# Performance work log

Hardware: AMD Instinct MI355X
Metric: run time of the kernel (lower is better)

The kernel has to match this reference:

```python
import jax, jax.numpy as jnp
import numpy as np

B, S, LATENT = 256, 64, 20
U_DIM = LATENT // 5            # 4
T_HID, T_DEPTH = 20, 4         # treatment MLP
D_HID, D_DEPTH = 4 * LATENT, 4 # drift MLP (80 hidden)
T_LEN = 41
DT = 0.05
SIGMA, THETA, MU = 0.5, 1.0, 0.0
N = B * S
DIM_AUG = LATENT + 2           # latent + logqp + Tx


def _mlp(x, w_in, b_in, w_h, b_h, w_out, b_out, act):
    # input layer always ReLU (MLPSimple), hidden layers use `act`
    h = jax.nn.relu(x @ w_in.T + b_in)
    for i in range(w_h.shape[0]):
        h = act(h @ w_h[i].T + b_h[i])
    return h @ w_out.T + b_out


def setup_inputs() -> dict:
    key = jax.random.key(0)
    ks = jax.random.split(key, 20)

    def lin(k, out_d, in_d):
        bound = 1.0 / np.sqrt(in_d)
        return jax.random.uniform(k, (out_d, in_d), jnp.float32, -bound, bound)

    def bias(k, out_d, in_d):
        bound = 1.0 / np.sqrt(in_d)
        return jax.random.uniform(k, (out_d,), jnp.float32, -bound, bound)

    return {
        "z_SDE": jax.random.normal(ks[0], (B, S, LATENT), jnp.float32),
        "t": jnp.arange(T_LEN, dtype=jnp.float32) * DT,
        "Tx": jax.random.uniform(ks[1], (B,), jnp.float32),
        "noise": jax.random.normal(ks[2], (T_LEN - 1, N, DIM_AUG), jnp.float32),
        # treatment MLP: 1 -> 20 (ReLU) -> [20->20 ReLU]x4 -> 4
        "tw_in": lin(ks[3], T_HID, 1),
        "tb_in": bias(ks[4], T_HID, 1),
        "tw_h": jnp.stack([lin(jax.random.fold_in(ks[5], i), T_HID, T_HID) for i in range(T_DEPTH)]),
        "tb_h": jnp.stack([bias(jax.random.fold_in(ks[6], i), T_HID, T_HID) for i in range(T_DEPTH)]),
        "tw_out": lin(ks[7], U_DIM, T_HID),
        "tb_out": bias(ks[8], U_DIM, T_HID),
        # drift MLP: 24 -> 80 (ReLU) -> [80->80 Tanh]x4 -> 20
        "dw_in": lin(ks[9], D_HID, LATENT + U_DIM),
        "db_in": bias(ks[10], D_HID, LATENT + U_DIM),
        "dw_h": jnp.stack([lin(jax.random.fold_in(ks[11], i), D_HID, D_HID) for i in range(D_DEPTH)]),
        "db_h": jnp.stack([bias(jax.random.fold_in(ks[12], i), D_HID, D_HID) for i in range(D_DEPTH)]),
        "dw_out": lin(ks[13], LATENT, D_HID),
        "db_out": bias(ks[14], LATENT, D_HID),
    }


def reference(z_SDE, t, Tx, noise, tw_in, tb_in, tw_h, tb_h, tw_out, tb_out,
              dw_in, db_in, dw_h, db_h, dw_out, db_out):
    # build augmented initial state: [z, logqp0=0, Tx]  -> [N, DIM_AUG]
    Tx_rep = jnp.broadcast_to(Tx[:, None, None], (B, S, 1))
    aug_y0 = jnp.concatenate(
        [z_SDE, jnp.zeros((B, S, 1), z_SDE.dtype), Tx_rep.astype(z_SDE.dtype)], axis=-1
    ).reshape(N, DIM_AUG)

    dt = t[1] - t[0]           # 0.05, aligned with euler dt
    sqrt_dt = jnp.sqrt(dt)
    # diagonal diffusion: sigma on latent dims, 0 on (logqp, Tx) aug dims
    g_diag = jnp.concatenate([jnp.full((LATENT,), SIGMA, jnp.float32), jnp.zeros((2,), jnp.float32)])

    def f_aug(ti, y_aug):
        T_ = y_aug[:, -1]                     # treatment indicator
        y = y_aug[:, :LATENT]
        t_col = jnp.broadcast_to(ti, (N, 1)).astype(y.dtype)
        u = _mlp(t_col, tw_in, tb_in, tw_h, tb_h, tw_out, tb_out, jax.nn.relu)
        u_t = u * T_[:, None]
        h = THETA * (MU - y)                  # prior drift
        f = _mlp(jnp.concatenate([y, u_t], axis=-1), dw_in, db_in, dw_h, db_h, dw_out, db_out, jnp.tanh) - h
        # _stable_division(f - h, g); g = sigma = 0.5 > eps so plain division
        uu = (f - h) / SIGMA
        f_logqp = 0.5 * jnp.sum(uu * uu, axis=1, keepdims=True)
        return jnp.concatenate([f, f_logqp, jnp.zeros_like(f_logqp)], axis=1)

    def step(y, inp):
        ti, dW = inp
        y_new = y + f_aug(ti, y) * dt + g_diag[None, :] * (dW * sqrt_dt)
        return y_new, y_new

    _, ys_rest = jax.lax.scan(step, aug_y0, (t[:-1], noise))
    aug_ys = jnp.concatenate([aug_y0[None], ys_rest], axis=0)   # [T, N, DIM_AUG]
    # faithful to source: raw reshape of [T, N, dim] into [B, S, T, dim]
    aug_ys = aug_ys.reshape(-1, S, T_LEN, DIM_AUG)
    ys = aug_ys[:, :, :, :-2]
    logqp = aug_ys[:, :, -1, -2]
    return ys, logqp
```

## Files before the change

### kernel.cpp

```cpp
#include <hip/hip_runtime.h>
#include <math.h>
#include <stdint.h>

#define NPART 16384
#define NSTEP 40
#define DIMA  22
#define OUT0_ELEMS 13434880
#define TRAJ_OFF   160

typedef __attribute__((ext_vector_type(8))) short short8;
typedef __attribute__((ext_vector_type(4))) float floatx4;
typedef __attribute__((ext_vector_type(4))) int   intx4;
typedef __attribute__((ext_vector_type(2))) int   intx2;

union V4 { intx4 i; short8 s; floatx4 f; };

#define AIN_B   0
#define AH_B    5120
#define AOUT_B  56320
#define U_B     61440
#define LDS_BYTES 62080
#define STAGE_DW  15360

__device__ __forceinline__ uint32_t bf16r(float x) {
    uint32_t u = __float_as_uint(x);
    u += 0x7FFFu + ((u >> 16) & 1u);
    return u >> 16;
}
__device__ __forceinline__ uint32_t pk2(float a0, float a1) {
    return bf16r(a0) | (bf16r(a1) << 16);
}
__device__ __forceinline__ float fast_tanh(float x) {
    float e = __expf(2.0f * x);
    return 1.0f - 2.0f * __builtin_amdgcn_rcpf(e + 1.0f);
}

__global__ __launch_bounds__(256, 1) void sde_mfma(
    const float* __restrict__ z,      const float* __restrict__ t_arr,
    const float* __restrict__ Tx,     const float* __restrict__ noise,
    const float* __restrict__ dw_in,  const float* __restrict__ db_in,
    const float* __restrict__ dw_h,   const float* __restrict__ db_h,
    const float* __restrict__ dw_out, const float* __restrict__ db_out,
    const float* __restrict__ tw_in,  const float* __restrict__ tb_in,
    const float* __restrict__ tw_h,   const float* __restrict__ tb_h,
    const float* __restrict__ tw_out, const float* __restrict__ tb_out,
    float* __restrict__ out0,         float* __restrict__ traj)
{
    __shared__ __align__(16) uint8_t lds[LDS_BYTES];
    const int tid = threadIdx.x;

    for (int di = tid; di < STAGE_DW; di += 256) {
        uint32_t val = 0u;
        if (di < 1280) {
            int r = di & 255, lane = r >> 2, w = r & 3;
            int m = lane & 15, q = lane >> 4, mt = di >> 8;
            int f = -1;
            if (w < 2)            f = 4 * q + 2 * w;
            else if (q == 0)      f = 16 + 2 * (w - 2);
            else if (q == 1)      f = 20 + 2 * (w - 2);
            if (f >= 0) val = pk2(dw_in[(mt * 16 + m) * 24 + f],
                                  dw_in[(mt * 16 + m) * 24 + f + 1]);
        } else if (di < 14080) {
            int q2 = di - 1280, g = q2 / 640, r = q2 % 640;
            int l = g / 5, mt = g % 5;
            int lane, f;
            if (r < 512) {
                int kt = r >> 8, rr = r & 255, w = rr & 3;
                lane = rr >> 2;
                f = 16 * (2 * kt + (w >> 1)) + 4 * (lane >> 4) + 2 * (w & 1);
            } else {
                int rr = r - 512, d = rr & 1;
                lane = rr >> 1;
                f = 64 + 4 * (lane >> 4) + 2 * d;
            }
            int m = lane & 15;
            val = pk2(dw_h[l * 6400 + (mt * 16 + m) * 80 + f],
                      dw_h[l * 6400 + (mt * 16 + m) * 80 + f + 1]);
        } else {
            int q2 = di - 14080, mt = q2 / 640, r = q2 % 640;
            int lane, f;
            if (r < 512) {
                int kt = r >> 8, rr = r & 255, w = rr & 3;
                lane = rr >> 2;
                f = 16 * (2 * kt + (w >> 1)) + 4 * (lane >> 4) + 2 * (w & 1);
            } else {
                int rr = r - 512, d = rr & 1;
                lane = rr >> 1;
                f = 64 + 4 * (lane >> 4) + 2 * d;
            }
            int m = mt * 16 + (lane & 15);
            if (m < 20) val = pk2(dw_out[m * 80 + f], dw_out[m * 80 + f + 1]);
        }
        ((uint32_t*)lds)[di] = val;
    }
    if (tid < NSTEP) {
        float ti = t_arr[tid];
        float hh[20], h2[20];
        #pragma unroll
        for (int j = 0; j < 20; j++) {
            float v = tw_in[j] * ti + tb_in[j];
            hh[j] = v > 0.f ? v : 0.f;
        }
        #pragma unroll
        for (int l = 0; l < 4; l++) {
            #pragma unroll
            for (int j = 0; j < 20; j++) {
                float a = tb_h[l * 20 + j];
                #pragma unroll
                for (int k = 0; k < 20; k++) a += tw_h[(l * 20 + j) * 20 + k] * hh[k];
                h2[j] = a > 0.f ? a : 0.f;
            }
            #pragma unroll
            for (int j = 0; j < 20; j++) hh[j] = h2[j];
        }
        #pragma unroll
        for (int c = 0; c < 4; c++) {
            float a = tb_out[c];
            #pragma unroll
            for (int k = 0; k < 20; k++) a += tw_out[c * 20 + k] * hh[k];
            ((float*)(lds + U_B))[tid * 4 + c] = a;
        }
    }

    const int lane = tid & 63;
    const int n15  = lane & 15;
    const int quad = lane >> 4;
    const int wv   = tid >> 6;
    const int n    = blockIdx.x * 64 + wv * 16 + n15;
    const float Txb = Tx[blockIdx.x];
    const float dtv = t_arr[1] - t_arr[0];
    const float sdt = sqrtf(dtv);

    floatx4 cIn[5], cH[4][5], cOut[2];
    #pragma unroll
    for (int mt = 0; mt < 5; mt++)
        cIn[mt] = *(const floatx4*)(db_in + mt * 16 + quad * 4);
    #pragma unroll
    for (int l = 0; l < 4; l++)
        #pragma unroll
        for (int mt = 0; mt < 5; mt++)
            cH[l][mt] = *(const floatx4*)(db_h + l * 80 + mt * 16 + quad * 4);
    cOut[0] = *(const floatx4*)(db_out + quad * 4);
    cOut[1] = (quad == 0) ? *(const floatx4*)(db_out + 16)
                          : (floatx4){0.f, 0.f, 0.f, 0.f};
    __syncthreads();

    float y0[4], y1[4] = {0.f, 0.f, 0.f, 0.f};
    {
        floatx4 zv = *(const floatx4*)(z + (size_t)n * 20 + quad * 4);
        #pragma unroll
        for (int r = 0; r < 4; r++) y0[r] = zv[r];
        *(floatx4*)(out0 + (size_t)n * 20 + quad * 4) = zv;
        if (quad == 0) {
            floatx4 z2 = *(const floatx4*)(z + (size_t)n * 20 + 16);
            #pragma unroll
            for (int r = 0; r < 4; r++) y1[r] = z2[r];
            *(floatx4*)(out0 + (size_t)n * 20 + 16) = z2;
            traj[n] = 0.f;
        }
    }

    double lq = 0.0;
    for (int i = 0; i < NSTEP; i++) {
        size_t nbase = ((size_t)i * NPART + n) * DIMA;
        floatx4 dW0 = *(const floatx4*)(noise + nbase + quad * 4);
        floatx4 dW1 = {0.f, 0.f, 0.f, 0.f};
        if (quad == 0) dW1 = *(const floatx4*)(noise + nbase + 16);

        const float* su = (const float*)(lds + U_B) + i * 4;
        float ut0 = su[0] * Txb, ut1 = su[1] * Txb;
        float ut2 = su[2] * Txb, ut3 = su[3] * Txb;

        V4 bin;
        bin.i[0] = pk2(y0[0], y0[1]);
        bin.i[1] = pk2(y0[2], y0[3]);
        if (quad == 0)      { bin.i[2] = pk2(y1[0], y1[1]); bin.i[3] = pk2(y1[2], y1[3]); }
        else if (quad == 1) { bin.i[2] = pk2(ut0, ut1);     bin.i[3] = pk2(ut2, ut3); }
        else                { bin.i[2] = 0;                 bin.i[3] = 0; }

        floatx4 acc[5];
        #pragma unroll
        for (int mt = 0; mt < 5; mt++) {
            V4 a; a.i = *(const intx4*)(lds + AIN_B + mt * 1024 + lane * 16);
            acc[mt] = __builtin_amdgcn_mfma_f32_16x16x32_bf16(a.s, bin.s, cIn[mt], 0, 0, 0);
        }
        uint32_t pkA[5][2];
        #pragma unroll
        for (int mt = 0; mt < 5; mt++) {
            pkA[mt][0] = pk2(fmaxf(acc[mt][0], 0.f), fmaxf(acc[mt][1], 0.f));
            pkA[mt][1] = pk2(fmaxf(acc[mt][2], 0.f), fmaxf(acc[mt][3], 0.f));
        }

        #pragma unroll
        for (int l = 0; l < 4; l++) {
            V4 b0, b1, b2;
            b0.i = (intx4){(int)pkA[0][0], (int)pkA[0][1], (int)pkA[1][0], (int)pkA[1][1]};
            b1.i = (intx4){(int)pkA[2][0], (int)pkA[2][1], (int)pkA[3][0], (int)pkA[3][1]};
            b2.i = (intx4){(int)pkA[4][0], (int)pkA[4][1], 0, 0};
            #pragma unroll
            for (int mt = 0; mt < 5; mt++) {
                const uint8_t* grp = lds + AH_B + (size_t)(l * 5 + mt) * 2560;
                V4 a0; a0.i = *(const intx4*)(grp + lane * 16);
                V4 a1; a1.i = *(const intx4*)(grp + 1024 + lane * 16);
                intx2 h2 = *(const intx2*)(grp + 2048 + lane * 8);
                V4 a2; a2.i = (intx4){h2[0], h2[1], 0, 0};
                floatx4 c = cH[l][mt];
                c = __builtin_amdgcn_mfma_f32_16x16x32_bf16(a0.s, b0.s, c, 0, 0, 0);
                c = __builtin_amdgcn_mfma_f32_16x16x32_bf16(a1.s, b1.s, c, 0, 0, 0);
                c = __builtin_amdgcn_mfma_f32_16x16x32_bf16(a2.s, b2.s, c, 0, 0, 0);
                acc[mt] = c;
            }
            #pragma unroll
            for (int mt = 0; mt < 5; mt++) {
                pkA[mt][0] = pk2(fast_tanh(acc[mt][0]), fast_tanh(acc[mt][1]));
                pkA[mt][1] = pk2(fast_tanh(acc[mt][2]), fast_tanh(acc[mt][3]));
            }
        }

        V4 b0, b1, b2;
        b0.i = (intx4){(int)pkA[0][0], (int)pkA[0][1], (int)pkA[1][0], (int)pkA[1][1]};
        b1.i = (intx4){(int)pkA[2][0], (int)pkA[2][1], (int)pkA[3][0], (int)pkA[3][1]};
        b2.i = (intx4){(int)pkA[4][0], (int)pkA[4][1], 0, 0};
        floatx4 oacc[2];
        #pragma unroll
        for (int mt = 0; mt < 2; mt++) {
            const uint8_t* grp = lds + AOUT_B + (size_t)mt * 2560;
            V4 a0; a0.i = *(const intx4*)(grp + lane * 16);
            V4 a1; a1.i = *(const intx4*)(grp + 1024 + lane * 16);
            intx2 h2 = *(const intx2*)(grp + 2048 + lane * 8);
            V4 a2; a2.i = (intx4){h2[0], h2[1], 0, 0};
            floatx4 c = cOut[mt];
            c = __builtin_amdgcn_mfma_f32_16x16x32_bf16(a0.s, b0.s, c, 0, 0, 0);
            c = __builtin_amdgcn_mfma_f32_16x16x32_bf16(a1.s, b1.s, c, 0, 0, 0);
            oacc[mt] = __builtin_amdgcn_mfma_f32_16x16x32_bf16(a2.s, b2.s, c, 0, 0, 0);
        }

        float part = 0.f;
        size_t obase = ((size_t)(i + 1) * NPART + n) * 20;
        floatx4 st;
        #pragma unroll
        for (int r = 0; r < 4; r++) {
            float o = oacc[0][r];
            float y = y0[r];
            float f = o + y;
            float uu = 2.f * o + 4.f * y;
            part += uu * uu;
            y0[r] = y + f * dtv + (0.5f * sdt) * dW0[r];
            st[r] = y0[r];
        }
        *(floatx4*)(out0 + obase + quad * 4) = st;
        if (quad == 0) {
            floatx4 st2;
            #pragma unroll
            for (int r = 0; r < 4; r++) {
                float o = oacc[1][r];
                float y = y1[r];
                float f = o + y;
                float uu = 2.f * o + 4.f * y;
                part += uu * uu;
                y1[r] = y + f * dtv + (0.5f * sdt) * dW1[r];
                st2[r] = y1[r];
            }
            *(floatx4*)(out0 + obase + 16) = st2;
        }
        part += __shfl_xor(part, 16);
        part += __shfl_xor(part, 32);
        lq += 0.5 * (double)part * (double)dtv;
        if (quad == 0) traj[(size_t)(i + 1) * NPART + n] = (float)lq;
    }
}

__global__ void gather_logqp(const float* __restrict__ traj, float* __restrict__ out1) {
    int i = blockIdx.x * 256 + threadIdx.x;
    if (i < NPART) out1[i] = traj[(size_t)41 * i + 40];
}

extern "C" void kernel_launch(void* const* d_in, const int* in_sizes, int n_in,
                              void* d_out, int out_size, void* d_ws, size_t ws_size,
                              hipStream_t stream) {
    const float* z      = (const float*)d_in[0];
    const float* t_arr  = (const float*)d_in[1];
    const float* Tx     = (const float*)d_in[2];
    const float* noise  = (const float*)d_in[3];
    const float* tw_in  = (const float*)d_in[4];
    const float* tb_in  = (const float*)d_in[5];
    const float* tw_h   = (const float*)d_in[6];
    const float* tb_h   = (const float*)d_in[7];
    const float* tw_out = (const float*)d_in[8];
    const float* tb_out = (const float*)d_in[9];
    const float* dw_in  = (const float*)d_in[10];
    const float* db_in  = (const float*)d_in[11];
    const float* dw_h   = (const float*)d_in[12];
    const float* db_h   = (const float*)d_in[13];
    const float* dw_out = (const float*)d_in[14];
    const float* db_out = (const float*)d_in[15];

    float* wsf  = (float*)d_ws;
    float* traj = wsf + TRAJ_OFF;
    float* out0 = (float*)d_out;
    float* out1 = out0 + OUT0_ELEMS;

    hipLaunchKernelGGL(sde_mfma, dim3(256), dim3(256), 0, stream,
                       z, t_arr, Tx, noise, dw_in, db_in, dw_h, db_h,
                       dw_out, db_out, tw_in, tb_in, tw_h, tb_h, tw_out, tb_out,
                       out0, traj);
    hipLaunchKernelGGL(gather_logqp, dim3(64), dim3(256), 0, stream, traj, out1);
}
```

Before: 274.8 us.

## Prefetch next layer weights from LDS, move biases to LDS, use packed bf16 convert

Bias vectors now live in LDS instead of about 88 persistent registers. The next MLP layer's weight fragments and biases are prefetched from LDS while the current layer's tanh is computed, so LDS latency overlaps with ALU work. The input-layer weights stay in registers across the time loop. The bf16 packing uses the hardware packed-convert builtin when it is available. This trades register pressure for extra LDS reads per step, and the packed convert may round differently in edge cases.

```diff
diff --git a/kernel.cpp b/kernel.cpp
--- a/kernel.cpp
+++ b/kernel.cpp
@@ -18,8 +18,8 @@
 #define AIN_B   0
 #define AH_B    5120
 #define AOUT_B  56320
-#define U_B     61440
-#define LDS_BYTES 62080
+#define SB_B    62080
+#define LDS_BYTES 64448
 #define STAGE_DW  15360
 
 __device__ __forceinline__ uint32_t bf16r(float x) {
@@ -29,6 +29,20 @@
 }
 __device__ __forceinline__ uint32_t pk2(float a0, float a1) {
     return bf16r(a0) | (bf16r(a1) << 16);
+}
+#if defined(__has_builtin)
+#if __has_builtin(__builtin_amdgcn_cvt_pk_bf16_f32)
+#define HAS_PKCVT 1
+#endif
+#endif
+__device__ __forceinline__ uint32_t pkq(float a0, float a1) {
+#ifdef HAS_PKCVT
+    auto r = __builtin_amdgcn_cvt_pk_bf16_f32(a0, a1);
+    uint32_t u; __builtin_memcpy(&u, &r, 4);
+    return u;
+#else
+    return pk2(a0, a1);
+#endif
 }
 __device__ __forceinline__ float fast_tanh(float x) {
     float e = __expf(2.0f * x);
@@ -93,32 +107,42 @@
         }
         ((uint32_t*)lds)[di] = val;
     }
-    if (tid < NSTEP) {
-        float ti = t_arr[tid];
-        float hh[20], h2[20];
-        #pragma unroll
-        for (int j = 0; j < 20; j++) {
-            float v = tw_in[j] * ti + tb_in[j];
-            hh[j] = v > 0.f ? v : 0.f;
-        }
-        #pragma unroll
-        for (int l = 0; l < 4; l++) {
+    {
+        float* sb = (float*)(lds + SB_B);
+        for (int di = tid; di < 432; di += 256) {
+            float v;
+            if (di < 80)       v = db_in[di];
+            else if (di < 400) v = db_h[di - 80];
+            else               v = (di - 400 < 20) ? db_out[di - 400] : 0.f;
+            sb[di] = v;
+        }
+        if (tid < NSTEP) {
+            float ti = t_arr[tid];
+            float hh[20], h2[20];
             #pragma unroll
             for (int j = 0; j < 20; j++) {
-                float a = tb_h[l * 20 + j];
-                #pragma unroll
-                for (int k = 0; k < 20; k++) a += tw_h[(l * 20 + j) * 20 + k] * hh[k];
-                h2[j] = a > 0.f ? a : 0.f;
-            }
-            #pragma unroll
-            for (int j = 0; j < 20; j++) hh[j] = h2[j];
-        }
-        #pragma unroll
-        for (int c = 0; c < 4; c++) {
-            float a = tb_out[c];
-            #pragma unroll
-            for (int k = 0; k < 20; k++) a += tw_out[c * 20 + k] * hh[k];
-            ((float*)(lds + U_B))[tid * 4 + c] = a;
+                float v = tw_in[j] * ti + tb_in[j];
+                hh[j] = v > 0.f ? v : 0.f;
+            }
+            #pragma unroll
+            for (int l = 0; l < 4; l++) {
+                #pragma unroll
+                for (int j = 0; j < 20; j++) {
+                    float a = tb_h[l * 20 + j];
+                    #pragma unroll
+                    for (int k = 0; k < 20; k++) a += tw_h[(l * 20 + j) * 20 + k] * hh[k];
+                    h2[j] = a > 0.f ? a : 0.f;
+                }
+                #pragma unroll
+                for (int j = 0; j < 20; j++) hh[j] = h2[j];
+            }
+            #pragma unroll
+            for (int c = 0; c < 4; c++) {
+                float a = tb_out[c];
+                #pragma unroll
+                for (int k = 0; k < 20; k++) a += tw_out[c * 20 + k] * hh[k];
+                sb[432 + tid * 4 + c] = a;
+            }
         }
     }
 
@@ -130,20 +154,13 @@
     const float Txb = Tx[blockIdx.x];
     const float dtv = t_arr[1] - t_arr[0];
     const float sdt = sqrtf(dtv);
-
-    floatx4 cIn[5], cH[4][5], cOut[2];
+    const float* sbf = (const float*)(lds + SB_B);
+    __syncthreads();
+
+    V4 aIn[5];
     #pragma unroll
     for (int mt = 0; mt < 5; mt++)
-        cIn[mt] = *(const floatx4*)(db_in + mt * 16 + quad * 4);
-    #pragma unroll
-    for (int l = 0; l < 4; l++)
-        #pragma unroll
-        for (int mt = 0; mt < 5; mt++)
-            cH[l][mt] = *(const floatx4*)(db_h + l * 80 + mt * 16 + quad * 4);
-    cOut[0] = *(const floatx4*)(db_out + quad * 4);
-    cOut[1] = (quad == 0) ? *(const floatx4*)(db_out + 16)
-                          : (floatx4){0.f, 0.f, 0.f, 0.f};
-    __syncthreads();
+        aIn[mt].i = *(const intx4*)(lds + AIN_B + mt * 1024 + lane * 16);
 
     float y0[4], y1[4] = {0.f, 0.f, 0.f, 0.f};
     {
@@ -167,30 +184,39 @@
         floatx4 dW1 = {0.f, 0.f, 0.f, 0.f};
         if (quad == 0) dW1 = *(const floatx4*)(noise + nbase + 16);
 
-        const float* su = (const float*)(lds + U_B) + i * 4;
-        float ut0 = su[0] * Txb, ut1 = su[1] * Txb;
-        float ut2 = su[2] * Txb, ut3 = su[3] * Txb;
+        float ut0 = sbf[432 + i * 4 + 0] * Txb, ut1 = sbf[432 + i * 4 + 1] * Txb;
+        float ut2 = sbf[432 + i * 4 + 2] * Txb, ut3 = sbf[432 + i * 4 + 3] * Txb;
 
         V4 bin;
-        bin.i[0] = pk2(y0[0], y0[1]);
-        bin.i[1] = pk2(y0[2], y0[3]);
-        if (quad == 0)      { bin.i[2] = pk2(y1[0], y1[1]); bin.i[3] = pk2(y1[2], y1[3]); }
-        else if (quad == 1) { bin.i[2] = pk2(ut0, ut1);     bin.i[3] = pk2(ut2, ut3); }
+        bin.i[0] = pkq(y0[0], y0[1]);
+        bin.i[1] = pkq(y0[2], y0[3]);
+        if (quad == 0)      { bin.i[2] = pkq(y1[0], y1[1]); bin.i[3] = pkq(y1[2], y1[3]); }
+        else if (quad == 1) { bin.i[2] = pkq(ut0, ut1);     bin.i[3] = pkq(ut2, ut3); }
         else                { bin.i[2] = 0;                 bin.i[3] = 0; }
 
         floatx4 acc[5];
         #pragma unroll
         for (int mt = 0; mt < 5; mt++) {
-            V4 a; a.i = *(const intx4*)(lds + AIN_B + mt * 1024 + lane * 16);
-            acc[mt] = __builtin_amdgcn_mfma_f32_16x16x32_bf16(a.s, bin.s, cIn[mt], 0, 0, 0);
+            floatx4 c = *(const floatx4*)(sbf + mt * 16 + quad * 4);
+            acc[mt] = __builtin_amdgcn_mfma_f32_16x16x32_bf16(aIn[mt].s, bin.s, c, 0, 0, 0);
+        }
+        V4 A0[5], A1[5]; intx2 A2[5]; floatx4 CB[5];
+        #pragma unroll
+        for (int mt = 0; mt < 5; mt++) {
+            const uint8_t* grp = lds + AH_B + (size_t)mt * 2560;
+            A0[mt].i = *(const intx4*)(grp + lane * 16);
+            A1[mt].i = *(const intx4*)(grp + 1024 + lane * 16);
+            A2[mt]   = *(const intx2*)(grp + 2048 + lane * 8);
+            CB[mt]   = *(const floatx4*)(sbf + 80 + mt * 16 + quad * 4);
         }
         uint32_t pkA[5][2];
         #pragma unroll
         for (int mt = 0; mt < 5; mt++) {
-            pkA[mt][0] = pk2(fmaxf(acc[mt][0], 0.f), fmaxf(acc[mt][1], 0.f));
-            pkA[mt][1] = pk2(fmaxf(acc[mt][2], 0.f), fmaxf(acc[mt][3], 0.f));
-        }
-
+            pkA[mt][0] = pkq(fmaxf(acc[mt][0], 0.f), fmaxf(acc[mt][1], 0.f));
+            pkA[mt][1] = pkq(fmaxf(acc[mt][2], 0.f), fmaxf(acc[mt][3], 0.f));
+        }
+
+        V4 O0[2], O1[2]; intx2 O2[2]; floatx4 OB[2];
         #pragma unroll
         for (int l = 0; l < 4; l++) {
             V4 b0, b1, b2;
@@ -199,21 +225,35 @@
             b2.i = (intx4){(int)pkA[4][0], (int)pkA[4][1], 0, 0};
             #pragma unroll
             for (int mt = 0; mt < 5; mt++) {
-                const uint8_t* grp = lds + AH_B + (size_t)(l * 5 + mt) * 2560;
-                V4 a0; a0.i = *(const intx4*)(grp + lane * 16);
-                V4 a1; a1.i = *(const intx4*)(grp + 1024 + lane * 16);
-                intx2 h2 = *(const intx2*)(grp + 2048 + lane * 8);
-                V4 a2; a2.i = (intx4){h2[0], h2[1], 0, 0};
-                floatx4 c = cH[l][mt];
-                c = __builtin_amdgcn_mfma_f32_16x16x32_bf16(a0.s, b0.s, c, 0, 0, 0);
-                c = __builtin_amdgcn_mfma_f32_16x16x32_bf16(a1.s, b1.s, c, 0, 0, 0);
-                c = __builtin_amdgcn_mfma_f32_16x16x32_bf16(a2.s, b2.s, c, 0, 0, 0);
-                acc[mt] = c;
+                V4 a2f; a2f.i = (intx4){A2[mt][0], A2[mt][1], 0, 0};
+                floatx4 c = CB[mt];
+                c = __builtin_amdgcn_mfma_f32_16x16x32_bf16(A0[mt].s, b0.s, c, 0, 0, 0);
+                c = __builtin_amdgcn_mfma_f32_16x16x32_bf16(A1[mt].s, b1.s, c, 0, 0, 0);
+                acc[mt] = __builtin_amdgcn_mfma_f32_16x16x32_bf16(a2f.s, b2.s, c, 0, 0, 0);
+            }
+            if (l < 3) {
+                #pragma unroll
+                for (int mt = 0; mt < 5; mt++) {
+                    const uint8_t* grp = lds + AH_B + (size_t)((l + 1) * 5 + mt) * 2560;
+                    A0[mt].i = *(const intx4*)(grp + lane * 16);
+                    A1[mt].i = *(const intx4*)(grp + 1024 + lane * 16);
+                    A2[mt]   = *(const intx2*)(grp + 2048 + lane * 8);
+                    CB[mt]   = *(const floatx4*)(sbf + 80 + (l + 1) * 80 + mt * 16 + quad * 4);
+                }
+            } else {
+                #pragma unroll
+                for (int mt = 0; mt < 2; mt++) {
+                    const uint8_t* grp = lds + AOUT_B + (size_t)mt * 2560;
+                    O0[mt].i = *(const intx4*)(grp + lane * 16);
+                    O1[mt].i = *(const intx4*)(grp + 1024 + lane * 16);
+                    O2[mt]   = *(const intx2*)(grp + 2048 + lane * 8);
+                    OB[mt]   = *(const floatx4*)(sbf + 400 + mt * 16 + quad * 4);
+                }
             }
             #pragma unroll
             for (int mt = 0; mt < 5; mt++) {
-                pkA[mt][0] = pk2(fast_tanh(acc[mt][0]), fast_tanh(acc[mt][1]));
-                pkA[mt][1] = pk2(fast_tanh(acc[mt][2]), fast_tanh(acc[mt][3]));
+                pkA[mt][0] = pkq(fast_tanh(acc[mt][0]), fast_tanh(acc[mt][1]));
+                pkA[mt][1] = pkq(fast_tanh(acc[mt][2]), fast_tanh(acc[mt][3]));
             }
         }
 
@@ -224,15 +264,11 @@
         floatx4 oacc[2];
         #pragma unroll
         for (int mt = 0; mt < 2; mt++) {
-            const uint8_t* grp = lds + AOUT_B + (size_t)mt * 2560;
-            V4 a0; a0.i = *(const intx4*)(grp + lane * 16);
-            V4 a1; a1.i = *(const intx4*)(grp + 1024 + lane * 16);
-            intx2 h2 = *(const intx2*)(grp + 2048 + lane * 8);
-            V4 a2; a2.i = (intx4){h2[0], h2[1], 0, 0};
-            floatx4 c = cOut[mt];
-            c = __builtin_amdgcn_mfma_f32_16x16x32_bf16(a0.s, b0.s, c, 0, 0, 0);
-            c = __builtin_amdgcn_mfma_f32_16x16x32_bf16(a1.s, b1.s, c, 0, 0, 0);
-            oacc[mt] = __builtin_amdgcn_mfma_f32_16x16x32_bf16(a2.s, b2.s, c, 0, 0, 0);
+            V4 a2f; a2f.i = (intx4){O2[mt][0], O2[mt][1], 0, 0};
+            floatx4 c = OB[mt];
+            c = __builtin_amdgcn_mfma_f32_16x16x32_bf16(O0[mt].s, b0.s, c, 0, 0, 0);
+            c = __builtin_amdgcn_mfma_f32_16x16x32_bf16(O1[mt].s, b1.s, c, 0, 0, 0);
+            oacc[mt] = __builtin_amdgcn_mfma_f32_16x16x32_bf16(a2f.s, b2.s, c, 0, 0, 0);
         }
 
         float part = 0.f;
```

Measured after the change: 277.2 us. About the same (+0.9%).
